# Kernel tuning notes

Hardware: AMD Instinct MI355X
Metric: run time of the kernel (lower is better)

Reference implementation:

```python
import jax, jax.numpy as jnp
import numpy as np

N = 200000      # nodes (1000 graphs x 200 nodes)
E = 1600000     # edges
N1 = 100000     # nodes after pool 1
E2 = 100000     # edges of pooled graph
N2 = 50000      # nodes after pool 2
B = 1000        # graphs
F_IN, C1, C2, H, NCLS = 1, 32, 64, 25, 10


def setup_inputs() -> dict:
    key = jax.random.key(0)
    ks = jax.random.split(key, 16)
    def lin(k, i, o):
        return jax.random.normal(k, (i, o), jnp.float32) / np.sqrt(i)
    inp = {
        'x': jax.random.normal(ks[0], (N, F_IN), jnp.float32),
        'pos': jax.random.uniform(ks[1], (N, 2), jnp.float32),
        'edge_index': jax.random.randint(ks[2], (2, E), 0, N, dtype=jnp.int32),
        'edge_attr': jax.random.uniform(ks[3], (E, 2), jnp.float32),
        'batch': (jnp.arange(N, dtype=jnp.int32) // (N // B)),
        'cluster1': (jnp.arange(N, dtype=jnp.int32) // 2),      # pairs of consecutive nodes -> same graph
        'edge_index2': jax.random.randint(ks[4], (2, E2), 0, N1, dtype=jnp.int32),
        'cluster2': (jnp.arange(N1, dtype=jnp.int32) // 2),
        'n1_w1': lin(ks[5], 2, H), 'n1_b1': jnp.zeros((H,), jnp.float32),
        'n1_w2': lin(ks[6], H, F_IN * C1), 'n1_b2': jnp.zeros((F_IN * C1,), jnp.float32),
        'root1': lin(ks[7], F_IN, C1), 'bias1': jnp.zeros((C1,), jnp.float32),
        'n2_w1': lin(ks[8], 2, H), 'n2_b1': jnp.zeros((H,), jnp.float32),
        'n2_w2': lin(ks[9], H, C1 * C2), 'n2_b2': jnp.zeros((C1 * C2,), jnp.float32),
        'root2': lin(ks[10], C1, C2), 'bias2': jnp.zeros((C2,), jnp.float32),
        'fc1_w': lin(ks[11], C2, 128), 'fc1_b': jnp.zeros((128,), jnp.float32),
        'fc2_w': lin(ks[12], 128, NCLS), 'fc2_b': jnp.zeros((NCLS,), jnp.float32),
    }
    return inp


def _cartesian(ei, pos):
    # PyG transforms.Cartesian(norm=True, cat=False)
    cart = pos[ei[0]] - pos[ei[1]]                      # [E, 2]
    m = jnp.max(jnp.abs(cart))
    return cart / (2.0 * m) + 0.5


def _nnconv(x, ei, ea, w1, b1, w2, b2, root, bias, n_nodes, c_in, c_out):
    # edge-conditioned weights: MLP(edge_attr) -> [E, c_in, c_out]
    w = (jax.nn.relu(ea @ w1 + b1) @ w2 + b2).reshape(-1, c_in, c_out)
    msg = jnp.einsum('ei,eio->eo', x[ei[0]], w)          # per-edge matmul with gathered src feats
    agg = jax.ops.segment_sum(msg, ei[1], num_segments=n_nodes)
    return agg + x @ root + bias


def _segment_mean(v, seg, n):
    s = jax.ops.segment_sum(v, seg, num_segments=n)
    c = jax.ops.segment_sum(jnp.ones((v.shape[0], 1), v.dtype), seg, num_segments=n)
    return s / jnp.maximum(c, 1.0)


def reference(x, pos, edge_index, edge_attr, batch, cluster1, edge_index2, cluster2,
              n1_w1, n1_b1, n1_w2, n1_b2, root1, bias1,
              n2_w1, n2_b1, n2_w2, n2_b2, root2, bias2,
              fc1_w, fc1_b, fc2_w, fc2_b):
    h = jax.nn.elu(_nnconv(x, edge_index, edge_attr, n1_w1, n1_b1, n1_w2, n1_b2,
                           root1, bias1, N, F_IN, C1))
    # max_pool(cluster1): segment-max feats, mean pos, carry batch; recompute Cartesian attrs
    x1 = jax.ops.segment_max(h, cluster1, num_segments=N1)
    pos1 = _segment_mean(pos, cluster1, N1)
    batch1 = jax.ops.segment_max(batch, cluster1, num_segments=N1)
    ea2 = _cartesian(edge_index2, pos1)
    h2 = jax.nn.elu(_nnconv(x1, edge_index2, ea2, n2_w1, n2_b1, n2_w2, n2_b2,
                            root2, bias2, N1, C1, C2))
    # max_pool_x(cluster2)
    x2 = jax.ops.segment_max(h2, cluster2, num_segments=N2)
    batch2 = jax.ops.segment_max(batch1, cluster2, num_segments=N2)
    g = _segment_mean(x2, batch2, B)                    # global_mean_pool -> [B, 64]
    z = jax.nn.elu(g @ fc1_w + fc1_b)                   # dropout is identity in eval
    return jax.nn.log_softmax(z @ fc2_w + fc2_b, axis=1)
```

## Files before the change

### kernel.cpp

```cpp
#include <hip/hip_runtime.h>
#include <hip/hip_bf16.h>

#define N_NODES 200000
#define E1 1600000
#define N1P 100000
#define E2P 100000
#define N2P 50000
#define BGR 1000
#define C1 32
#define C2 64
#define HIDN 25
#define NCLS 10

typedef short short8 __attribute__((ext_vector_type(8)));
typedef int int4v __attribute__((ext_vector_type(4)));
typedef float f32x4 __attribute__((ext_vector_type(4)));
typedef float f32x2 __attribute__((ext_vector_type(2)));

union FragU { int4v i; short8 s; };

__device__ __forceinline__ float elu1(float v) {
    return v > 0.f ? v : expm1f(v);
}
__device__ __forceinline__ float bf2f(unsigned short u) {
    return __uint_as_float(((unsigned int)u) << 16);
}
__device__ __forceinline__ unsigned int pk_bf16(float a, float b) {
    unsigned int r;
    asm("v_cvt_pk_bf16_f32 %0, %1, %2" : "=v"(r) : "v"(a), "v"(b));
    return r;
}
__device__ __forceinline__ void atomic_pk_bf16(unsigned short* p, unsigned int pk) {
    asm volatile("global_atomic_pk_add_bf16 %0, %1, off" :: "v"(p), "v"(pk) : "memory");
}

__global__ __launch_bounds__(256) void bgbuild_kernel(
    const float* __restrict__ w2a, const float* __restrict__ b2a,
    const float* __restrict__ w2b, const float* __restrict__ b2b,
    const float* __restrict__ pos, const int* __restrict__ ei2,
    unsigned int* __restrict__ W2f, unsigned int* __restrict__ Bg,
    unsigned int* __restrict__ maxbits)
{
    int blk = blockIdx.x, t = threadIdx.x;
    if (blk < 2) {
        int q = blk * 256 + t;
        int jj = q & 3, l = (q >> 2) & 63, m = q >> 8;
        int k0 = (l >> 4) * 8 + 2 * jj;
        int o = 2 * (l & 15) + m;
        float v0 = (k0 < 25) ? w2a[k0 * 32 + o] : (k0 == 25 ? b2a[o] : 0.f);
        int k1 = k0 + 1;
        float v1 = (k1 < 25) ? w2a[k1 * 32 + o] : (k1 == 25 ? b2a[o] : 0.f);
        W2f[q] = pk_bf16(v0, v1);
    } else {
        int idx = (blk - 2) * 256 + t;
        if (idx < 26 * 4 * 64 * 4) {
            int g0 = idx * 2;
            int j = g0 & 7;
            int l = (g0 >> 3) & 63;
            int nb = (g0 >> 9) & 3;
            int kt = g0 >> 11;
            int k = kt * 32 + (l >> 4) * 8 + j;
            int o = (nb >> 1) * 32 + 2 * (l & 15) + (nb & 1);
            float v0, v1;
            if (k < 800) { v0 = w2b[k * 64 + o]; v1 = w2b[(k + 1) * 64 + o]; }
            else         { v0 = b2b[(k - 800) * 64 + o]; v1 = b2b[(k - 799) * 64 + o]; }
            Bg[idx] = pk_bf16(v0, v1);
        }
    }
    float m = 0.f;
    for (int e = blk * 256 + t; e < E2P; e += gridDim.x * 256) {
        int s = ei2[e], d = ei2[E2P + e];
        f32x2 ps0 = ((const f32x2*)pos)[2 * s], ps1 = ((const f32x2*)pos)[2 * s + 1];
        f32x2 pd0 = ((const f32x2*)pos)[2 * d], pd1 = ((const f32x2*)pos)[2 * d + 1];
        float c0 = 0.5f * (ps0.x + ps1.x) - 0.5f * (pd0.x + pd1.x);
        float c1 = 0.5f * (ps0.y + ps1.y) - 0.5f * (pd0.y + pd1.y);
        m = fmaxf(m, fmaxf(fabsf(c0), fabsf(c1)));
    }
#pragma unroll
    for (int off = 32; off; off >>= 1)
        m = fmaxf(m, __shfl_down(m, off));
    if ((t & 63) == 0)
        atomicMax(maxbits, __float_as_uint(m));
}

__global__ __launch_bounds__(256) void conv1_kernel(
    const float* __restrict__ x, const float* __restrict__ ea,
    const int* __restrict__ ei,
    const float* __restrict__ w1, const float* __restrict__ b1,
    const unsigned int* __restrict__ W2f,
    unsigned short* __restrict__ agg1b)
{
    __shared__ unsigned int afrag[16][4][64];
    __shared__ int dst_lds[256];

    int t = threadIdx.x;
    int e = blockIdx.x * 256 + t;
    f32x2 a = ((const f32x2*)ea)[e];
    int s = ei[e], d = ei[E1 + e];
    float xv = x[s];
    dst_lds[t] = d;

    float v[26];
#pragma unroll
    for (int h = 0; h < HIDN; ++h) {
        float u = fmaf(a.x, w1[h], fmaf(a.y, w1[HIDN + h], b1[h]));
        v[h] = fmaxf(u, 0.f) * xv;
    }
    v[25] = xv;

    int tile = t >> 4, r16 = t & 15;
#pragma unroll
    for (int p = 0; p < 13; ++p) {
        int g = p >> 2, j = p & 3;
        afrag[tile][j][g * 16 + r16] = pk_bf16(v[2 * p], v[2 * p + 1]);
    }
    afrag[tile][1][48 + r16] = 0;
    afrag[tile][2][48 + r16] = 0;
    afrag[tile][3][48 + r16] = 0;
    __syncthreads();

    int lane = t & 63, wave = t >> 6;
    FragU bf0, bf1;
    bf0.i = *(const int4v*)(W2f + lane * 4);
    bf1.i = *(const int4v*)(W2f + (64 + lane) * 4);
    int c = lane & 15, rg = lane >> 4;

#pragma unroll
    for (int ti = 0; ti < 4; ++ti) {
        int tl = wave * 4 + ti;
        FragU af;
        af.i.x = afrag[tl][0][lane];
        af.i.y = afrag[tl][1][lane];
        af.i.z = afrag[tl][2][lane];
        af.i.w = afrag[tl][3][lane];
        f32x4 a0 = (f32x4){0.f, 0.f, 0.f, 0.f};
        f32x4 a1 = (f32x4){0.f, 0.f, 0.f, 0.f};
        a0 = __builtin_amdgcn_mfma_f32_16x16x32_bf16(af.s, bf0.s, a0, 0, 0, 0);
        a1 = __builtin_amdgcn_mfma_f32_16x16x32_bf16(af.s, bf1.s, a1, 0, 0, 0);
#pragma unroll
        for (int jj = 0; jj < 4; ++jj) {
            int le = tl * 16 + rg * 4 + jj;
            atomic_pk_bf16(agg1b + (size_t)dst_lds[le] * C1 + 2 * c,
                           pk_bf16(a0[jj], a1[jj]));
        }
    }
}

__global__ __launch_bounds__(256) void pool1_kernel(
    const unsigned short* __restrict__ agg1b, const float* __restrict__ x,
    const float* __restrict__ root1, const float* __restrict__ bias1,
    unsigned short* __restrict__ x1b)
{
    int t = blockIdx.x * blockDim.x + threadIdx.x;
    if (t >= N1P * C1) return;
    int j = t >> 5, o = t & 31;
    int na = 2 * j, nb = 2 * j + 1;
    float r = root1[o], bo = bias1[o];
    float ha = elu1(bf2f(agg1b[(size_t)na * C1 + o]) + x[na] * r + bo);
    float hb = elu1(bf2f(agg1b[(size_t)nb * C1 + o]) + x[nb] * r + bo);
    float mx = fmaxf(ha, hb);
    x1b[t] = (unsigned short)(pk_bf16(mx, mx) & 0xffffu);
}

__global__ __launch_bounds__(256) void conv2_kernel(
    const int* __restrict__ ei2, const float* __restrict__ pos,
    const unsigned short* __restrict__ x1b,
    const float* __restrict__ w1, const float* __restrict__ b1,
    const unsigned int* __restrict__ maxbits,
    const unsigned int* __restrict__ Bg,
    unsigned short* __restrict__ agg2b)
{
    __shared__ __align__(16) unsigned short xs_lds[128][40];
    __shared__ unsigned int hidb[128][14];
    __shared__ int dst_lds[128];

    int t = threadIdx.x;
    int base = blockIdx.x * 128;

    if (t < 128) {
        int ge = base + t;
        bool ok = ge < E2P;
        float inv = 0.5f / __uint_as_float(maxbits[0]);
        int s = 0, d = 0;
        if (ok) { s = ei2[ge]; d = ei2[E2P + ge]; }
        dst_lds[t] = d;
        f32x2 ps0 = ((const f32x2*)pos)[2 * s], ps1 = ((const f32x2*)pos)[2 * s + 1];
        f32x2 pd0 = ((const f32x2*)pos)[2 * d], pd1 = ((const f32x2*)pos)[2 * d + 1];
        float a0 = (0.5f * (ps0.x + ps1.x) - 0.5f * (pd0.x + pd1.x)) * inv + 0.5f;
        float a1 = (0.5f * (ps0.y + ps1.y) - 0.5f * (pd0.y + pd1.y)) * inv + 0.5f;
        float hv[26];
#pragma unroll
        for (int h = 0; h < HIDN; ++h) {
            float u = fmaf(a0, w1[h], fmaf(a1, w1[HIDN + h], b1[h]));
            hv[h] = ok ? fmaxf(u, 0.f) : 0.f;
        }
        hv[25] = 0.f;
#pragma unroll
        for (int p = 0; p < 13; ++p)
            hidb[t][p] = pk_bf16(hv[2 * p], hv[2 * p + 1]);
        const int4v* xp = (const int4v*)(x1b + (size_t)s * C1);
#pragma unroll
        for (int q = 0; q < 4; ++q) {
            int4v z4 = (int4v){0, 0, 0, 0};
            *(int4v*)&xs_lds[t][q * 8] = ok ? xp[q] : z4;
        }
    }
    __syncthreads();

    int lane = t & 63, wave = t >> 6;
    int c = lane & 15, rg = lane >> 4;

    FragU xv2[2];
    float xfl[2][8];
#pragma unroll
    for (int ti = 0; ti < 2; ++ti) {
        int row = (wave * 2 + ti) * 16 + c;
        xv2[ti].i = *(const int4v*)&xs_lds[row][rg * 8];
#pragma unroll
        for (int g2 = 0; g2 < 4; ++g2) {
            unsigned int u = (unsigned int)xv2[ti].i[g2];
            xfl[ti][2 * g2]     = __uint_as_float(u << 16);
            xfl[ti][2 * g2 + 1] = __uint_as_float(u & 0xffff0000u);
        }
    }

    f32x4 acc[2][4];
#pragma unroll
    for (int ti = 0; ti < 2; ++ti)
#pragma unroll
        for (int nb = 0; nb < 4; ++nb)
            acc[ti][nb] = (f32x4){0.f, 0.f, 0.f, 0.f};

    const int4v* Bg4 = (const int4v*)Bg;
    FragU bf[4];
#pragma unroll
    for (int nb = 0; nb < 4; ++nb)
        bf[nb].i = Bg4[nb * 64 + lane];

#pragma unroll
    for (int kt = 0; kt < 25; ++kt) {
        FragU bn[4];
#pragma unroll
        for (int nb = 0; nb < 4; ++nb)
            bn[nb].i = Bg4[((kt + 1) * 4 + nb) * 64 + lane];
#pragma unroll
        for (int ti = 0; ti < 2; ++ti) {
            unsigned int hu = hidb[(wave * 2 + ti) * 16 + c][kt >> 1];
            float hvv = bf2f((unsigned short)((kt & 1) ? (hu >> 16) : (hu & 0xffffu)));
            FragU af;
            af.i.x = pk_bf16(hvv * xfl[ti][0], hvv * xfl[ti][1]);
            af.i.y = pk_bf16(hvv * xfl[ti][2], hvv * xfl[ti][3]);
            af.i.z = pk_bf16(hvv * xfl[ti][4], hvv * xfl[ti][5]);
            af.i.w = pk_bf16(hvv * xfl[ti][6], hvv * xfl[ti][7]);
#pragma unroll
            for (int nb = 0; nb < 4; ++nb)
                acc[ti][nb] = __builtin_amdgcn_mfma_f32_16x16x32_bf16(af.s, bf[nb].s, acc[ti][nb], 0, 0, 0);
        }
#pragma unroll
        for (int nb = 0; nb < 4; ++nb) bf[nb] = bn[nb];
    }
#pragma unroll
    for (int ti = 0; ti < 2; ++ti)
#pragma unroll
        for (int nb = 0; nb < 4; ++nb)
            acc[ti][nb] = __builtin_amdgcn_mfma_f32_16x16x32_bf16(xv2[ti].s, bf[nb].s, acc[ti][nb], 0, 0, 0);

#pragma unroll
    for (int ti = 0; ti < 2; ++ti) {
        int tl = wave * 2 + ti;
#pragma unroll
        for (int jj = 0; jj < 4; ++jj) {
            int le = tl * 16 + rg * 4 + jj;
            if (base + le < E2P) {
                unsigned short* dp = agg2b + (size_t)dst_lds[le] * C2;
                atomic_pk_bf16(dp + 2 * c,      pk_bf16(acc[ti][0][jj], acc[ti][1][jj]));
                atomic_pk_bf16(dp + 32 + 2 * c, pk_bf16(acc[ti][2][jj], acc[ti][3][jj]));
            }
        }
    }
}

__global__ __launch_bounds__(256) void pool2_head_kernel(
    const unsigned short* __restrict__ agg2b, const unsigned short* __restrict__ x1b,
    const float* __restrict__ root2, const float* __restrict__ bias2,
    const float* __restrict__ fc1w, const float* __restrict__ fc1b,
    const float* __restrict__ fc2w, const float* __restrict__ fc2b,
    float* __restrict__ out)
{
    int b = blockIdx.x;
    int t = threadIdx.x;
    int w = t >> 6, o = t & 63;
    __shared__ float part[4][C2];
    __shared__ float gs[C2];
    __shared__ float zs[128];
    __shared__ float ls[NCLS];

    float r2[C1];
#pragma unroll
    for (int i = 0; i < C1; ++i) r2[i] = root2[i * C2 + o];
    float bo = bias2[o];

    float sum = 0.f;
    for (int jj = w; jj < 50; jj += 4) {
        int j = b * 50 + jj;
        float hv[2];
#pragma unroll
        for (int tt = 0; tt < 2; ++tt) {
            int n = 2 * j + tt;
            float a = bf2f(agg2b[(size_t)n * C2 + o]) + bo;
            const int4v* xp = (const int4v*)(x1b + (size_t)n * C1);
#pragma unroll
            for (int q = 0; q < 4; ++q) {
                int4v v4 = xp[q];
#pragma unroll
                for (int g2 = 0; g2 < 4; ++g2) {
                    unsigned int u = (unsigned int)v4[g2];
                    a = fmaf(__uint_as_float(u << 16),         r2[q * 8 + 2 * g2],     a);
                    a = fmaf(__uint_as_float(u & 0xffff0000u), r2[q * 8 + 2 * g2 + 1], a);
                }
            }
            hv[tt] = elu1(a);
        }
        sum += fmaxf(hv[0], hv[1]);
    }
    part[w][o] = sum;
    __syncthreads();
    if (w == 0)
        gs[o] = (part[0][o] + part[1][o] + part[2][o] + part[3][o]) * (1.f / 50.f);
    __syncthreads();
    if (t < 128) {
        float z = fc1b[t];
#pragma unroll
        for (int i = 0; i < C2; ++i) z = fmaf(gs[i], fc1w[i * 128 + t], z);
        zs[t] = elu1(z);
    }
    __syncthreads();
    if (t < NCLS) {
        float l = fc2b[t];
#pragma unroll
        for (int k = 0; k < 128; ++k) l = fmaf(zs[k], fc2w[k * NCLS + t], l);
        ls[t] = l;
    }
    __syncthreads();
    if (t < NCLS) {
        float mx = ls[0];
#pragma unroll
        for (int cc = 1; cc < NCLS; ++cc) mx = fmaxf(mx, ls[cc]);
        float se = 0.f;
#pragma unroll
        for (int cc = 0; cc < NCLS; ++cc) se += expf(ls[cc] - mx);
        out[b * NCLS + t] = ls[t] - mx - logf(se);
    }
}

extern "C" void kernel_launch(void* const* d_in, const int* in_sizes, int n_in,
                              void* d_out, int out_size, void* d_ws, size_t ws_size,
                              hipStream_t stream)
{
    const float* x    = (const float*)d_in[0];
    const float* pos  = (const float*)d_in[1];
    const int*   ei   = (const int*)d_in[2];
    const float* ea   = (const float*)d_in[3];
    const int*   ei2  = (const int*)d_in[6];
    const float* n1w1 = (const float*)d_in[8];
    const float* n1b1 = (const float*)d_in[9];
    const float* n1w2 = (const float*)d_in[10];
    const float* n1b2 = (const float*)d_in[11];
    const float* root1= (const float*)d_in[12];
    const float* bias1= (const float*)d_in[13];
    const float* n2w1 = (const float*)d_in[14];
    const float* n2b1 = (const float*)d_in[15];
    const float* n2w2 = (const float*)d_in[16];
    const float* n2b2 = (const float*)d_in[17];
    const float* root2= (const float*)d_in[18];
    const float* bias2= (const float*)d_in[19];
    const float* fc1w = (const float*)d_in[20];
    const float* fc1b = (const float*)d_in[21];
    const float* fc2w = (const float*)d_in[22];
    const float* fc2b = (const float*)d_in[23];
    float* out = (float*)d_out;

    char* w = (char*)d_ws;
    unsigned short* agg1b = (unsigned short*)w;  w += (size_t)N_NODES * C1 * 2;
    unsigned short* agg2b = (unsigned short*)w;  w += (size_t)N1P * C2 * 2;
    unsigned int* maxbits = (unsigned int*)w;    w += 1024;
    size_t zero_bytes = (size_t)N_NODES * C1 * 2 + (size_t)N1P * C2 * 2 + 1024;
    unsigned short* x1b   = (unsigned short*)w;  w += (size_t)N1P * C1 * 2;
    unsigned int* Bg = (unsigned int*)w;         w += 26624 * 4;
    unsigned int* W2f = (unsigned int*)w;        w += 512 * 4;

    hipMemsetAsync(agg1b, 0, zero_bytes, stream);

    bgbuild_kernel<<<106, 256, 0, stream>>>(n1w2, n1b2, n2w2, n2b2, pos, ei2,
                                            W2f, Bg, maxbits);
    conv1_kernel<<<E1 / 256, 256, 0, stream>>>(x, ea, ei, n1w1, n1b1, W2f, agg1b);
    pool1_kernel<<<(N1P * C1 + 255) / 256, 256, 0, stream>>>(agg1b, x, root1, bias1, x1b);
    conv2_kernel<<<(E2P + 127) / 128, 256, 0, stream>>>(ei2, pos, x1b, n2w1, n2b1, maxbits, Bg, agg2b);
    pool2_head_kernel<<<BGR, 256, 0, stream>>>(agg2b, x1b, root2, bias2,
                                               fc1w, fc1b, fc2w, fc2b, out);
}
```

Measured before the change: 165.3 us.

## Fold weight-prep kernel into conv1 and pool1, widen conv2 to 256 edges per block

Removes the separate bgbuild launch. Each conv1 block now builds its own bf16 W2 fragment in shared memory, and the Bg weight build plus the pos max-reduction run as extra blocks appended to the pool1 grid. conv2 now handles 256 edges per block with all threads doing edge prep, each wave owning four 16-edge tiles, and the k-loop no longer unrolled. This cuts one launch and halves the conv2 grid in exchange for redundant W2 prep in every conv1 block and higher register and LDS pressure in conv2.

```diff
diff --git a/kernel.cpp b/kernel.cpp
--- a/kernel.cpp
+++ b/kernel.cpp
@@ -11,6 +11,8 @@
 #define C2 64
 #define HIDN 25
 #define NCLS 10
+#define POOL1_BLKS 12500
+#define BG_BLKS 104
 
 typedef short short8 __attribute__((ext_vector_type(8)));
 typedef int int4v __attribute__((ext_vector_type(4)));
@@ -34,26 +36,96 @@
     asm volatile("global_atomic_pk_add_bf16 %0, %1, off" :: "v"(p), "v"(pk) : "memory");
 }
 
-__global__ __launch_bounds__(256) void bgbuild_kernel(
+__global__ __launch_bounds__(256) void conv1_kernel(
+    const float* __restrict__ x, const float* __restrict__ ea,
+    const int* __restrict__ ei,
+    const float* __restrict__ w1, const float* __restrict__ b1,
     const float* __restrict__ w2a, const float* __restrict__ b2a,
-    const float* __restrict__ w2b, const float* __restrict__ b2b,
-    const float* __restrict__ pos, const int* __restrict__ ei2,
-    unsigned int* __restrict__ W2f, unsigned int* __restrict__ Bg,
-    unsigned int* __restrict__ maxbits)
+    unsigned short* __restrict__ agg1b)
 {
-    int blk = blockIdx.x, t = threadIdx.x;
-    if (blk < 2) {
-        int q = blk * 256 + t;
+    __shared__ unsigned int afrag[16][4][64];
+    __shared__ int dst_lds[256];
+    __shared__ unsigned int w2f[512];
+
+    int t = threadIdx.x;
+#pragma unroll
+    for (int half = 0; half < 2; ++half) {
+        int q = half * 256 + t;
         int jj = q & 3, l = (q >> 2) & 63, m = q >> 8;
         int k0 = (l >> 4) * 8 + 2 * jj;
         int o = 2 * (l & 15) + m;
         float v0 = (k0 < 25) ? w2a[k0 * 32 + o] : (k0 == 25 ? b2a[o] : 0.f);
         int k1 = k0 + 1;
         float v1 = (k1 < 25) ? w2a[k1 * 32 + o] : (k1 == 25 ? b2a[o] : 0.f);
-        W2f[q] = pk_bf16(v0, v1);
-    } else {
-        int idx = (blk - 2) * 256 + t;
-        if (idx < 26 * 4 * 64 * 4) {
+        w2f[q] = pk_bf16(v0, v1);
+    }
+
+    int e = blockIdx.x * 256 + t;
+    f32x2 a = ((const f32x2*)ea)[e];
+    int s = ei[e], d = ei[E1 + e];
+    float xv = x[s];
+    dst_lds[t] = d;
+
+    float v[26];
+#pragma unroll
+    for (int h = 0; h < HIDN; ++h) {
+        float u = fmaf(a.x, w1[h], fmaf(a.y, w1[HIDN + h], b1[h]));
+        v[h] = fmaxf(u, 0.f) * xv;
+    }
+    v[25] = xv;
+
+    int tile = t >> 4, r16 = t & 15;
+#pragma unroll
+    for (int p = 0; p < 13; ++p) {
+        int g = p >> 2, j = p & 3;
+        afrag[tile][j][g * 16 + r16] = pk_bf16(v[2 * p], v[2 * p + 1]);
+    }
+    afrag[tile][1][48 + r16] = 0;
+    afrag[tile][2][48 + r16] = 0;
+    afrag[tile][3][48 + r16] = 0;
+    __syncthreads();
+
+    int lane = t & 63, wave = t >> 6;
+    FragU bf0, bf1;
+    bf0.i = *(const int4v*)(w2f + lane * 4);
+    bf1.i = *(const int4v*)(w2f + (64 + lane) * 4);
+    int c = lane & 15, rg = lane >> 4;
+
+#pragma unroll
+    for (int ti = 0; ti < 4; ++ti) {
+        int tl = wave * 4 + ti;
+        FragU af;
+        af.i.x = afrag[tl][0][lane];
+        af.i.y = afrag[tl][1][lane];
+        af.i.z = afrag[tl][2][lane];
+        af.i.w = afrag[tl][3][lane];
+        f32x4 a0 = (f32x4){0.f, 0.f, 0.f, 0.f};
+        f32x4 a1 = (f32x4){0.f, 0.f, 0.f, 0.f};
+        a0 = __builtin_amdgcn_mfma_f32_16x16x32_bf16(af.s, bf0.s, a0, 0, 0, 0);
+        a1 = __builtin_amdgcn_mfma_f32_16x16x32_bf16(af.s, bf1.s, a1, 0, 0, 0);
+#pragma unroll
+        for (int jj = 0; jj < 4; ++jj) {
+            int le = tl * 16 + rg * 4 + jj;
+            atomic_pk_bf16(agg1b + (size_t)dst_lds[le] * C1 + 2 * c,
+                           pk_bf16(a0[jj], a1[jj]));
+        }
+    }
+}
+
+__global__ __launch_bounds__(256) void pool1_kernel(
+    const unsigned short* __restrict__ agg1b, const float* __restrict__ x,
+    const float* __restrict__ root1, const float* __restrict__ bias1,
+    unsigned short* __restrict__ x1b,
+    const float* __restrict__ w2b, const float* __restrict__ b2b,
+    const float* __restrict__ pos, const int* __restrict__ ei2,
+    unsigned int* __restrict__ Bg, unsigned int* __restrict__ maxbits)
+{
+    int bid = blockIdx.x;
+    int t = threadIdx.x;
+    if (bid >= POOL1_BLKS) {
+        int blk2 = bid - POOL1_BLKS;
+        {
+            int idx = blk2 * 256 + t;
             int g0 = idx * 2;
             int j = g0 & 7;
             int l = (g0 >> 3) & 63;
@@ -66,100 +138,30 @@
             else         { v0 = b2b[(k - 800) * 64 + o]; v1 = b2b[(k - 799) * 64 + o]; }
             Bg[idx] = pk_bf16(v0, v1);
         }
-    }
-    float m = 0.f;
-    for (int e = blk * 256 + t; e < E2P; e += gridDim.x * 256) {
-        int s = ei2[e], d = ei2[E2P + e];
-        f32x2 ps0 = ((const f32x2*)pos)[2 * s], ps1 = ((const f32x2*)pos)[2 * s + 1];
-        f32x2 pd0 = ((const f32x2*)pos)[2 * d], pd1 = ((const f32x2*)pos)[2 * d + 1];
-        float c0 = 0.5f * (ps0.x + ps1.x) - 0.5f * (pd0.x + pd1.x);
-        float c1 = 0.5f * (ps0.y + ps1.y) - 0.5f * (pd0.y + pd1.y);
-        m = fmaxf(m, fmaxf(fabsf(c0), fabsf(c1)));
-    }
-#pragma unroll
-    for (int off = 32; off; off >>= 1)
-        m = fmaxf(m, __shfl_down(m, off));
-    if ((t & 63) == 0)
-        atomicMax(maxbits, __float_as_uint(m));
-}
-
-__global__ __launch_bounds__(256) void conv1_kernel(
-    const float* __restrict__ x, const float* __restrict__ ea,
-    const int* __restrict__ ei,
-    const float* __restrict__ w1, const float* __restrict__ b1,
-    const unsigned int* __restrict__ W2f,
-    unsigned short* __restrict__ agg1b)
-{
-    __shared__ unsigned int afrag[16][4][64];
-    __shared__ int dst_lds[256];
-
-    int t = threadIdx.x;
-    int e = blockIdx.x * 256 + t;
-    f32x2 a = ((const f32x2*)ea)[e];
-    int s = ei[e], d = ei[E1 + e];
-    float xv = x[s];
-    dst_lds[t] = d;
-
-    float v[26];
-#pragma unroll
-    for (int h = 0; h < HIDN; ++h) {
-        float u = fmaf(a.x, w1[h], fmaf(a.y, w1[HIDN + h], b1[h]));
-        v[h] = fmaxf(u, 0.f) * xv;
-    }
-    v[25] = xv;
-
-    int tile = t >> 4, r16 = t & 15;
-#pragma unroll
-    for (int p = 0; p < 13; ++p) {
-        int g = p >> 2, j = p & 3;
-        afrag[tile][j][g * 16 + r16] = pk_bf16(v[2 * p], v[2 * p + 1]);
-    }
-    afrag[tile][1][48 + r16] = 0;
-    afrag[tile][2][48 + r16] = 0;
-    afrag[tile][3][48 + r16] = 0;
-    __syncthreads();
-
-    int lane = t & 63, wave = t >> 6;
-    FragU bf0, bf1;
-    bf0.i = *(const int4v*)(W2f + lane * 4);
-    bf1.i = *(const int4v*)(W2f + (64 + lane) * 4);
-    int c = lane & 15, rg = lane >> 4;
-
-#pragma unroll
-    for (int ti = 0; ti < 4; ++ti) {
-        int tl = wave * 4 + ti;
-        FragU af;
-        af.i.x = afrag[tl][0][lane];
-        af.i.y = afrag[tl][1][lane];
-        af.i.z = afrag[tl][2][lane];
-        af.i.w = afrag[tl][3][lane];
-        f32x4 a0 = (f32x4){0.f, 0.f, 0.f, 0.f};
-        f32x4 a1 = (f32x4){0.f, 0.f, 0.f, 0.f};
-        a0 = __builtin_amdgcn_mfma_f32_16x16x32_bf16(af.s, bf0.s, a0, 0, 0, 0);
-        a1 = __builtin_amdgcn_mfma_f32_16x16x32_bf16(af.s, bf1.s, a1, 0, 0, 0);
-#pragma unroll
-        for (int jj = 0; jj < 4; ++jj) {
-            int le = tl * 16 + rg * 4 + jj;
-            atomic_pk_bf16(agg1b + (size_t)dst_lds[le] * C1 + 2 * c,
-                           pk_bf16(a0[jj], a1[jj]));
-        }
-    }
-}
-
-__global__ __launch_bounds__(256) void pool1_kernel(
-    const unsigned short* __restrict__ agg1b, const float* __restrict__ x,
-    const float* __restrict__ root1, const float* __restrict__ bias1,
-    unsigned short* __restrict__ x1b)
-{
-    int t = blockIdx.x * blockDim.x + threadIdx.x;
-    if (t >= N1P * C1) return;
-    int j = t >> 5, o = t & 31;
+        float m = 0.f;
+        for (int e = blk2 * 256 + t; e < E2P; e += BG_BLKS * 256) {
+            int s = ei2[e], d = ei2[E2P + e];
+            f32x2 ps0 = ((const f32x2*)pos)[2 * s], ps1 = ((const f32x2*)pos)[2 * s + 1];
+            f32x2 pd0 = ((const f32x2*)pos)[2 * d], pd1 = ((const f32x2*)pos)[2 * d + 1];
+            float c0 = 0.5f * (ps0.x + ps1.x) - 0.5f * (pd0.x + pd1.x);
+            float c1 = 0.5f * (ps0.y + ps1.y) - 0.5f * (pd0.y + pd1.y);
+            m = fmaxf(m, fmaxf(fabsf(c0), fabsf(c1)));
+        }
+#pragma unroll
+        for (int off = 32; off; off >>= 1)
+            m = fmaxf(m, __shfl_down(m, off));
+        if ((t & 63) == 0)
+            atomicMax(maxbits, __float_as_uint(m));
+        return;
+    }
+    int tt = bid * 256 + t;
+    int j = tt >> 5, o = tt & 31;
     int na = 2 * j, nb = 2 * j + 1;
     float r = root1[o], bo = bias1[o];
     float ha = elu1(bf2f(agg1b[(size_t)na * C1 + o]) + x[na] * r + bo);
     float hb = elu1(bf2f(agg1b[(size_t)nb * C1 + o]) + x[nb] * r + bo);
     float mx = fmaxf(ha, hb);
-    x1b[t] = (unsigned short)(pk_bf16(mx, mx) & 0xffffu);
+    x1b[tt] = (unsigned short)(pk_bf16(mx, mx) & 0xffffu);
 }
 
 __global__ __launch_bounds__(256) void conv2_kernel(
@@ -170,14 +172,14 @@
     const unsigned int* __restrict__ Bg,
     unsigned short* __restrict__ agg2b)
 {
-    __shared__ __align__(16) unsigned short xs_lds[128][40];
-    __shared__ unsigned int hidb[128][14];
-    __shared__ int dst_lds[128];
+    __shared__ __align__(16) unsigned short xs_lds[256][40];
+    __shared__ unsigned int hidb[256][14];
+    __shared__ int dst_lds[256];
 
     int t = threadIdx.x;
-    int base = blockIdx.x * 128;
-
-    if (t < 128) {
+    int base = blockIdx.x * 256;
+
+    {
         int ge = base + t;
         bool ok = ge < E2P;
         float inv = 0.5f / __uint_as_float(maxbits[0]);
@@ -210,23 +212,23 @@
     int lane = t & 63, wave = t >> 6;
     int c = lane & 15, rg = lane >> 4;
 
-    FragU xv2[2];
-    float xfl[2][8];
-#pragma unroll
-    for (int ti = 0; ti < 2; ++ti) {
-        int row = (wave * 2 + ti) * 16 + c;
-        xv2[ti].i = *(const int4v*)&xs_lds[row][rg * 8];
+    FragU xv4[4];
+    float xfl[4][8];
+#pragma unroll
+    for (int ti = 0; ti < 4; ++ti) {
+        int row = (wave * 4 + ti) * 16 + c;
+        xv4[ti].i = *(const int4v*)&xs_lds[row][rg * 8];
 #pragma unroll
         for (int g2 = 0; g2 < 4; ++g2) {
-            unsigned int u = (unsigned int)xv2[ti].i[g2];
+            unsigned int u = (unsigned int)xv4[ti].i[g2];
             xfl[ti][2 * g2]     = __uint_as_float(u << 16);
             xfl[ti][2 * g2 + 1] = __uint_as_float(u & 0xffff0000u);
         }
     }
 
-    f32x4 acc[2][4];
-#pragma unroll
-    for (int ti = 0; ti < 2; ++ti)
+    f32x4 acc[4][4];
+#pragma unroll
+    for (int ti = 0; ti < 4; ++ti)
 #pragma unroll
         for (int nb = 0; nb < 4; ++nb)
             acc[ti][nb] = (f32x4){0.f, 0.f, 0.f, 0.f};
@@ -237,15 +239,15 @@
     for (int nb = 0; nb < 4; ++nb)
         bf[nb].i = Bg4[nb * 64 + lane];
 
-#pragma unroll
+#pragma unroll 1
     for (int kt = 0; kt < 25; ++kt) {
         FragU bn[4];
 #pragma unroll
         for (int nb = 0; nb < 4; ++nb)
             bn[nb].i = Bg4[((kt + 1) * 4 + nb) * 64 + lane];
 #pragma unroll
-        for (int ti = 0; ti < 2; ++ti) {
-            unsigned int hu = hidb[(wave * 2 + ti) * 16 + c][kt >> 1];
+        for (int ti = 0; ti < 4; ++ti) {
+            unsigned int hu = hidb[(wave * 4 + ti) * 16 + c][kt >> 1];
             float hvv = bf2f((unsigned short)((kt & 1) ? (hu >> 16) : (hu & 0xffffu)));
             FragU af;
             af.i.x = pk_bf16(hvv * xfl[ti][0], hvv * xfl[ti][1]);
@@ -260,14 +262,14 @@
         for (int nb = 0; nb < 4; ++nb) bf[nb] = bn[nb];
     }
 #pragma unroll
-    for (int ti = 0; ti < 2; ++ti)
+    for (int ti = 0; ti < 4; ++ti)
 #pragma unroll
         for (int nb = 0; nb < 4; ++nb)
-            acc[ti][nb] = __builtin_amdgcn_mfma_f32_16x16x32_bf16(xv2[ti].s, bf[nb].s, acc[ti][nb], 0, 0, 0);
-
-#pragma unroll
-    for (int ti = 0; ti < 2; ++ti) {
-        int tl = wave * 2 + ti;
+            acc[ti][nb] = __builtin_amdgcn_mfma_f32_16x16x32_bf16(xv4[ti].s, bf[nb].s, acc[ti][nb], 0, 0, 0);
+
+#pragma unroll
+    for (int ti = 0; ti < 4; ++ti) {
+        int tl = wave * 4 + ti;
 #pragma unroll
         for (int jj = 0; jj < 4; ++jj) {
             int le = tl * 16 + rg * 4 + jj;
@@ -387,15 +389,13 @@
     size_t zero_bytes = (size_t)N_NODES * C1 * 2 + (size_t)N1P * C2 * 2 + 1024;
     unsigned short* x1b   = (unsigned short*)w;  w += (size_t)N1P * C1 * 2;
     unsigned int* Bg = (unsigned int*)w;         w += 26624 * 4;
-    unsigned int* W2f = (unsigned int*)w;        w += 512 * 4;
 
     hipMemsetAsync(agg1b, 0, zero_bytes, stream);
 
-    bgbuild_kernel<<<106, 256, 0, stream>>>(n1w2, n1b2, n2w2, n2b2, pos, ei2,
-                                            W2f, Bg, maxbits);
-    conv1_kernel<<<E1 / 256, 256, 0, stream>>>(x, ea, ei, n1w1, n1b1, W2f, agg1b);
-    pool1_kernel<<<(N1P * C1 + 255) / 256, 256, 0, stream>>>(agg1b, x, root1, bias1, x1b);
-    conv2_kernel<<<(E2P + 127) / 128, 256, 0, stream>>>(ei2, pos, x1b, n2w1, n2b1, maxbits, Bg, agg2b);
+    conv1_kernel<<<E1 / 256, 256, 0, stream>>>(x, ea, ei, n1w1, n1b1, n1w2, n1b2, agg1b);
+    pool1_kernel<<<POOL1_BLKS + BG_BLKS, 256, 0, stream>>>(agg1b, x, root1, bias1, x1b,
+                                                           n2w2, n2b2, pos, ei2, Bg, maxbits);
+    conv2_kernel<<<(E2P + 255) / 256, 256, 0, stream>>>(ei2, pos, x1b, n2w1, n2b1, maxbits, Bg, agg2b);
     pool2_head_kernel<<<BGR, 256, 0, stream>>>(agg2b, x1b, root2, bias2,
                                                fc1w, fc1b, fc2w, fc2b, out);
 }
```

Measured after the change: 159.7 us. 1.04x faster.
